# Performance work log

Measured on AMD Instinct MI355X. Metric: run time of the kernel, lower is better.

Reference implementation:

```python
import jax, jax.numpy as jnp
import numpy as np

NEG_SLOPE = 0.2  # PyG GATConv default negative_slope


def _gat_edge_forward(x, edge_index, edge_attr, W, W_edge, att_src, att_dst, att_edge, bias):
    N = x.shape[0]
    H, C = att_src.shape
    src, dst = edge_index[0], edge_index[1]

    # --- add self loops with edge_attr fill_value='mean' (PyG default) ---
    ones = jnp.ones((edge_attr.shape[0],), dtype=x.dtype)
    cnt = jax.ops.segment_sum(ones, dst, num_segments=N)  # [N]
    attr_sum = jax.ops.segment_sum(edge_attr, dst, num_segments=N)  # [N, edge_dim]
    loop_attr = attr_sum / jnp.maximum(cnt, 1.0)[:, None]  # mean, 0 if no in-edges
    loop_idx = jnp.arange(N, dtype=edge_index.dtype)
    src_all = jnp.concatenate([src, loop_idx])
    dst_all = jnp.concatenate([dst, loop_idx])
    attr_all = jnp.concatenate([edge_attr, loop_attr], axis=0)  # [E+N, edge_dim]

    # --- linear projections ---
    x_l = (x @ W).reshape(N, H, C)  # [N,H,C]; GATConv uses same lin for src/dst
    a_src = jnp.einsum('nhc,hc->nh', x_l, att_src)  # [N,H]
    a_dst = jnp.einsum('nhc,hc->nh', x_l, att_dst)  # [N,H]
    e = (attr_all @ W_edge).reshape(-1, H, C)  # [E+N,H,C]
    a_edge = jnp.einsum('ehc,hc->eh', e, att_edge)  # [E+N,H]

    # --- per-edge attention logits + segment softmax over incoming edges ---
    logits = jax.nn.leaky_relu(a_src[src_all] + a_dst[dst_all] + a_edge, NEG_SLOPE)
    m = jax.ops.segment_max(logits, dst_all, num_segments=N)  # [N,H]
    p = jnp.exp(logits - m[dst_all])
    denom = jax.ops.segment_sum(p, dst_all, num_segments=N)  # [N,H]
    alpha = p / denom[dst_all]  # [E+N,H]

    # --- weighted scatter aggregation ---
    msgs = alpha[:, :, None] * x_l[src_all]  # [E+N,H,C]
    out = jax.ops.segment_sum(msgs, dst_all, num_segments=N)  # [N,H,C]
    return out.reshape(N, H * C) + bias  # concat=True -> [N, H*C]


def setup_inputs() -> dict:
    key = jax.random.key(0)
    ks = jax.random.split(key, 8)
    N, E, DIN, EDIM, H, C = 100000, 1600000, 128, 16, 4, 32
    s = 1.0 / np.sqrt(DIN)
    return {
        'x': jax.random.normal(ks[0], (N, DIN), jnp.float32),
        'edge_index': jax.random.randint(ks[1], (2, E), 0, N, jnp.int64),
        'edge_attr': jax.random.normal(ks[2], (E, EDIM), jnp.float32),
        'W': jax.random.normal(ks[3], (DIN, H * C), jnp.float32) * s,
        'W_edge': jax.random.normal(ks[4], (EDIM, H * C), jnp.float32) * (1.0 / np.sqrt(EDIM)),
        'att_src': jax.random.normal(ks[5], (H, C), jnp.float32) * 0.1,
        'att_dst': jax.random.normal(ks[6], (H, C), jnp.float32) * 0.1,
        'att_edge': jax.random.normal(ks[7], (H, C), jnp.float32) * 0.1,
        'bias': jnp.zeros((H * C,), jnp.float32),
    }


def reference(x, edge_index, edge_attr, W, W_edge, att_src, att_dst, att_edge, bias):
    return _gat_edge_forward(x, edge_index, edge_attr, W, W_edge, att_src, att_dst, att_edge, bias)
```

## Files before the change

kernel.cpp:

```cpp
#include <hip/hip_runtime.h>
#include <hip/hip_fp16.h>
#include <math.h>

#define NEG_SLOPE 0.2f
typedef unsigned short ushort_t;
typedef unsigned int uint_t;

__global__ void k_prep(const int* __restrict__ ei, int* __restrict__ is64,
                       int* __restrict__ deg, int N,
                       const float* __restrict__ W_edge, const float* __restrict__ att_edge,
                       float* __restrict__ v_edge) {
  int b = blockIdx.x, t = threadIdx.x;
  if (b == 0) {
    __shared__ int any;
    if (t == 0) any = 0;
    __syncthreads();
    if (ei[2 * t + 1] != 0) atomicOr(&any, 1);
    __syncthreads();
    if (t == 0) *is64 = (any == 0) ? 1 : 0;
  } else if (b == 1) {
    if (t < 64) {
      int h = t >> 4, j = t & 15;
      float s = 0.f;
#pragma unroll
      for (int c = 0; c < 32; ++c) s += W_edge[j * 128 + h * 32 + c] * att_edge[h * 32 + c];
      v_edge[t] = s;
    }
  } else {
    int i = (b - 2) * 256 + t;
    if (i < N) deg[i] = 0;
  }
}

__global__ void k_hist(const int* __restrict__ ei, const int* __restrict__ is64,
                       int* __restrict__ deg, int* __restrict__ rank, int E) {
  int i = blockIdx.x * blockDim.x + threadIdx.x;
  if (i >= E) return;
  int dst = (*is64) ? ei[2 * (E + i)] : ei[E + i];
  rank[i] = atomicAdd(&deg[dst], 1);
}

__global__ void k_scan1(const int* __restrict__ deg, int* __restrict__ bsum, int N) {
  __shared__ int lds[256];
  int b = blockIdx.x, t = threadIdx.x;
  int base = b * 1024 + t * 4;
  int s = 0;
  if (base + 3 < N) {
    int4 v = *(const int4*)&deg[base];
    s = v.x + v.y + v.z + v.w;
  } else {
    for (int q = 0; q < 4; ++q) if (base + q < N) s += deg[base + q];
  }
  lds[t] = s; __syncthreads();
  for (int st = 128; st > 0; st >>= 1) {
    if (t < st) lds[t] += lds[t + st];
    __syncthreads();
  }
  if (t == 0) bsum[b] = lds[0];
}

__global__ void k_scan2(const int* __restrict__ bsum, int* __restrict__ boff, int NB) {
  __shared__ int lds[256];
  int t = threadIdx.x;
  int v = (t < NB) ? bsum[t] : 0;
  lds[t] = v;
  __syncthreads();
  for (int st = 1; st < 256; st <<= 1) {
    int add = (t >= st) ? lds[t - st] : 0;
    __syncthreads();
    lds[t] += add;
    __syncthreads();
  }
  if (t < NB) boff[t] = lds[t] - v;
}

__global__ void k_scan3(const int* __restrict__ deg, const int* __restrict__ boff,
                        int* __restrict__ offs, int N) {
  __shared__ int lds[256];
  int b = blockIdx.x, t = threadIdx.x;
  int base = b * 1024 + t * 4;
  int v[4]; int s = 0;
#pragma unroll
  for (int q = 0; q < 4; ++q) { v[q] = (base + q < N) ? deg[base + q] : 0; s += v[q]; }
  lds[t] = s;
  __syncthreads();
  for (int st = 1; st < 256; st <<= 1) {
    int add = (t >= st) ? lds[t - st] : 0;
    __syncthreads();
    lds[t] += add;
    __syncthreads();
  }
  int run = boff[b] + lds[t] - s;
#pragma unroll
  for (int q = 0; q < 4; ++q) {
    if (base + q < N) offs[base + q] = run;
    run += v[q];
  }
}

__global__ __launch_bounds__(256) void k1_scatter(
    const float* __restrict__ x, const float* __restrict__ W,
    const float* __restrict__ att_src, const float* __restrict__ att_dst,
    ushort_t* __restrict__ x_l_h, float* __restrict__ a_src, float* __restrict__ a_dst, int N,
    const int* __restrict__ ei, const int* __restrict__ is64,
    const int* __restrict__ rank, const int* __restrict__ offs,
    const float* __restrict__ edge_attr, const float* __restrict__ v_edge,
    int4* __restrict__ rec, int E, int nbs) {
  __shared__ float Wc[32 * 128];
  __shared__ float Xc[32 * 64];
  const int t = threadIdx.x;
  if (blockIdx.x < nbs) {
    if (t < 64) Wc[t] = v_edge[t];
    __syncthreads();
    int i = blockIdx.x * 256 + t;
    if (i >= E) return;
    int f = *is64;
    int src = f ? ei[2 * i] : ei[i];
    int dst = f ? ei[2 * (E + i)] : ei[E + i];
    float a16[16];
    *(float4*)&a16[0]  = *(const float4*)&edge_attr[(size_t)i * 16];
    *(float4*)&a16[4]  = *(const float4*)&edge_attr[(size_t)i * 16 + 4];
    *(float4*)&a16[8]  = *(const float4*)&edge_attr[(size_t)i * 16 + 8];
    *(float4*)&a16[12] = *(const float4*)&edge_attr[(size_t)i * 16 + 12];
    float ae[4];
#pragma unroll
    for (int h = 0; h < 4; ++h) {
      float s = 0.f;
#pragma unroll
      for (int j = 0; j < 16; ++j) s += a16[j] * Wc[h * 16 + j];
      ae[h] = s;
    }
    int pos = offs[dst] + rank[i];
    __half2 e01 = __floats2half2_rn(ae[0], ae[1]);
    __half2 e23 = __floats2half2_rn(ae[2], ae[3]);
    int4 r; r.x = *(int*)&e01; r.y = *(int*)&e23; r.z = src; r.w = 0;
    rec[pos] = r;
    return;
  }
  const int tcol = t & 31;
  const int trow = t >> 5;
  const int row0 = (blockIdx.x - nbs) * 64;
  const int r = t & 63, kq = t >> 6;
  const float4 aw_s = *(const float4*)&att_src[tcol * 4];
  const float4 aw_d = *(const float4*)&att_dst[tcol * 4];
  float acc[8][4];
#pragma unroll
  for (int i = 0; i < 8; ++i) { acc[i][0] = acc[i][1] = acc[i][2] = acc[i][3] = 0.f; }

  for (int kc = 0; kc < 4; ++kc) {
    float4 wreg[4];
#pragma unroll
    for (int q = 0; q < 4; ++q) wreg[q] = *(const float4*)&W[kc * 4096 + (q * 256 + t) * 4];
    float xs8[8];
    int grow = row0 + r;
    if (grow < N) {
      *(float4*)&xs8[0] = *(const float4*)&x[grow * 128 + kc * 32 + kq * 8];
      *(float4*)&xs8[4] = *(const float4*)&x[grow * 128 + kc * 32 + kq * 8 + 4];
    } else {
#pragma unroll
      for (int q = 0; q < 8; ++q) xs8[q] = 0.f;
    }
    __syncthreads();
#pragma unroll
    for (int q = 0; q < 4; ++q) *(float4*)&Wc[(q * 256 + t) * 4] = wreg[q];
#pragma unroll
    for (int q = 0; q < 8; ++q) Xc[(kq * 8 + q) * 64 + r] = xs8[q];
    __syncthreads();
#pragma unroll
    for (int kk = 0; kk < 32; ++kk) {
      float4 wv = *(const float4*)&Wc[kk * 128 + tcol * 4];
      float xr[8];
      *(float4*)&xr[0] = *(const float4*)&Xc[kk * 64 + trow * 8];
      *(float4*)&xr[4] = *(const float4*)&Xc[kk * 64 + trow * 8 + 4];
#pragma unroll
      for (int ri = 0; ri < 8; ++ri) {
        acc[ri][0] += xr[ri] * wv.x;
        acc[ri][1] += xr[ri] * wv.y;
        acc[ri][2] += xr[ri] * wv.z;
        acc[ri][3] += xr[ri] * wv.w;
      }
    }
  }
#pragma unroll
  for (int ri = 0; ri < 8; ++ri) {
    int grow = row0 + trow * 8 + ri;
    float asp = acc[ri][0] * aw_s.x + acc[ri][1] * aw_s.y + acc[ri][2] * aw_s.z + acc[ri][3] * aw_s.w;
    float adp = acc[ri][0] * aw_d.x + acc[ri][1] * aw_d.y + acc[ri][2] * aw_d.z + acc[ri][3] * aw_d.w;
#pragma unroll
    for (int m = 1; m < 8; m <<= 1) { asp += __shfl_xor(asp, m); adp += __shfl_xor(adp, m); }
    if (grow < N) {
      __half2 h0 = __floats2half2_rn(acc[ri][0], acc[ri][1]);
      __half2 h1 = __floats2half2_rn(acc[ri][2], acc[ri][3]);
      uint2 u; u.x = *(uint_t*)&h0; u.y = *(uint_t*)&h1;
      *(uint2*)&x_l_h[(size_t)grow * 128 + tcol * 4] = u;
      if ((tcol & 7) == 0) {
        a_src[grow * 4 + (tcol >> 3)] = asp;
        a_dst[grow * 4 + (tcol >> 3)] = adp;
      }
    }
  }
}

__global__ __launch_bounds__(256) void k34_agg(
    const int4* __restrict__ rec, const uint_t* __restrict__ xu,
    const float* __restrict__ a_src, const float* __restrict__ a_dst,
    const int* __restrict__ deg, const int* __restrict__ offs,
    const float* __restrict__ bias, float* __restrict__ out, int N) {
  int lane = threadIdx.x & 63;
  int node = blockIdx.x * 4 + (threadIdx.x >> 6);
  if (node >= N) return;
  int offu = __builtin_amdgcn_readfirstlane(offs[node]);
  int dgu  = __builtin_amdgcn_readfirstlane(deg[node]);
  const int4* rp = rec + offu;
  int h = lane >> 4;
  int hs16 = (h & 1) << 4;
  float ad = a_dst[(size_t)node * 4 + h];
  float accx = 0.f, accy = 0.f, den = 0.f, sae = 0.f;
  int i = 0;
  for (; i + 4 <= dgu; i += 4) {
    int4 u0 = rp[i], u1 = rp[i + 1], u2 = rp[i + 2], u3 = rp[i + 3];
    int s0 = __builtin_amdgcn_readfirstlane(u0.z);
    int s1 = __builtin_amdgcn_readfirstlane(u1.z);
    int s2 = __builtin_amdgcn_readfirstlane(u2.z);
    int s3 = __builtin_amdgcn_readfirstlane(u3.z);
    uint_t v0 = xu[((size_t)(uint_t)s0 << 6) + lane];
    uint_t v1 = xu[((size_t)(uint_t)s1 << 6) + lane];
    uint_t v2 = xu[((size_t)(uint_t)s2 << 6) + lane];
    uint_t v3 = xu[((size_t)(uint_t)s3 << 6) + lane];
    float as0 = a_src[((size_t)(uint_t)s0 << 2) + h];
    float as1 = a_src[((size_t)(uint_t)s1 << 2) + h];
    float as2 = a_src[((size_t)(uint_t)s2 << 2) + h];
    float as3 = a_src[((size_t)(uint_t)s3 << 2) + h];
    uint_t w0 = (h & 2) ? (uint_t)u0.y : (uint_t)u0.x;
    uint_t w1 = (h & 2) ? (uint_t)u1.y : (uint_t)u1.x;
    uint_t w2 = (h & 2) ? (uint_t)u2.y : (uint_t)u2.x;
    uint_t w3 = (h & 2) ? (uint_t)u3.y : (uint_t)u3.x;
    float e0 = __half2float(__ushort_as_half((ushort_t)(w0 >> hs16)));
    float e1 = __half2float(__ushort_as_half((ushort_t)(w1 >> hs16)));
    float e2 = __half2float(__ushort_as_half((ushort_t)(w2 >> hs16)));
    float e3 = __half2float(__ushort_as_half((ushort_t)(w3 >> hs16)));
    float g0 = as0 + ad + e0; g0 = fmaxf(g0, NEG_SLOPE * g0);
    float g1 = as1 + ad + e1; g1 = fmaxf(g1, NEG_SLOPE * g1);
    float g2 = as2 + ad + e2; g2 = fmaxf(g2, NEG_SLOPE * g2);
    float g3 = as3 + ad + e3; g3 = fmaxf(g3, NEG_SLOPE * g3);
    float p0 = __expf(g0), p1 = __expf(g1), p2 = __expf(g2), p3 = __expf(g3);
    den += p0 + p1 + p2 + p3;
    sae += e0 + e1 + e2 + e3;
    float2 f0 = __half22float2(*(const __half2*)&v0);
    float2 f1 = __half22float2(*(const __half2*)&v1);
    float2 f2 = __half22float2(*(const __half2*)&v2);
    float2 f3 = __half22float2(*(const __half2*)&v3);
    accx += p0 * f0.x; accy += p0 * f0.y;
    accx += p1 * f1.x; accy += p1 * f1.y;
    accx += p2 * f2.x; accy += p2 * f2.y;
    accx += p3 * f3.x; accy += p3 * f3.y;
  }
  for (; i < dgu; ++i) {
    int4 u = rp[i];
    int s = __builtin_amdgcn_readfirstlane(u.z);
    uint_t v = xu[((size_t)(uint_t)s << 6) + lane];
    float as = a_src[((size_t)(uint_t)s << 2) + h];
    uint_t w = (h & 2) ? (uint_t)u.y : (uint_t)u.x;
    float e = __half2float(__ushort_as_half((ushort_t)(w >> hs16)));
    float g = as + ad + e; g = fmaxf(g, NEG_SLOPE * g);
    float p = __expf(g);
    den += p; sae += e;
    float2 fx = __half22float2(*(const __half2*)&v);
    accx += p * fx.x; accy += p * fx.y;
  }
  float asn = a_src[(size_t)node * 4 + h];
  float inv_cnt = 1.f / (float)(dgu > 0 ? dgu : 1);
  float gl = asn + ad + sae * inv_cnt;
  gl = fmaxf(gl, NEG_SLOPE * gl);
  float pl = __expf(gl);
  float iv = 1.f / (den + pl);
  uint_t vn = xu[((size_t)(uint_t)node << 6) + lane];
  float2 fn = __half22float2(*(const __half2*)&vn);
  float2 b2 = *(const float2*)&bias[2 * lane];
  float2 o;
  o.x = (accx + pl * fn.x) * iv + b2.x;
  o.y = (accy + pl * fn.y) * iv + b2.y;
  *(float2*)&out[(size_t)node * 128 + 2 * lane] = o;
}

extern "C" void kernel_launch(void* const* d_in, const int* in_sizes, int n_in,
                              void* d_out, int out_size, void* d_ws, size_t ws_size,
                              hipStream_t stream) {
  const float* x        = (const float*)d_in[0];
  const int*   ei       = (const int*)  d_in[1];
  const float* eattr    = (const float*)d_in[2];
  const float* W        = (const float*)d_in[3];
  const float* W_edge   = (const float*)d_in[4];
  const float* att_src  = (const float*)d_in[5];
  const float* att_dst  = (const float*)d_in[6];
  const float* att_edge = (const float*)d_in[7];
  const float* bias     = (const float*)d_in[8];
  float* out = (float*)d_out;
  const int N = in_sizes[0] / 128;
  const int E = in_sizes[1] / 2;
  (void)n_in; (void)out_size; (void)ws_size;

  char* base = (char*)d_ws;
  size_t off = 0;
  auto take = [&](size_t bytes) -> void* {
    void* p = base + off;
    off = (off + bytes + 255) & ~(size_t)255;
    return p;
  };
  ushort_t* x_l_h = (ushort_t*)take((size_t)N * 128 * 2);
  float* a_src    = (float*)take((size_t)N * 4 * 4);
  float* a_dst    = (float*)take((size_t)N * 4 * 4);
  float* v_edge   = (float*)take(64 * 4);
  int4*  rec      = (int4*)take((size_t)E * 16);
  int*   deg      = (int*)take((size_t)N * 4);
  int*   offs     = (int*)take((size_t)N * 4);
  int*   rank     = (int*)take((size_t)E * 4);
  int*   bsum     = (int*)take(256 * 4);
  int*   boff     = (int*)take(256 * 4);
  int*   is64     = (int*)take(4);

  const int NB = (N + 1023) / 1024;
  const int nbs = (E + 255) / 256;
  const int nb1 = (N + 63) / 64;

  hipLaunchKernelGGL(k_prep, dim3(2 + (N + 255) / 256), dim3(256), 0, stream,
                     ei, is64, deg, N, W_edge, att_edge, v_edge);
  hipLaunchKernelGGL(k_hist, dim3(nbs), dim3(256), 0, stream, ei, is64, deg, rank, E);
  hipLaunchKernelGGL(k_scan1, dim3(NB), dim3(256), 0, stream, deg, bsum, N);
  hipLaunchKernelGGL(k_scan2, dim3(1), dim3(256), 0, stream, bsum, boff, NB);
  hipLaunchKernelGGL(k_scan3, dim3(NB), dim3(256), 0, stream, deg, boff, offs, N);
  hipLaunchKernelGGL(k1_scatter, dim3(nbs + nb1), dim3(256), 0, stream,
                     x, W, att_src, att_dst, x_l_h, a_src, a_dst, N,
                     ei, is64, rank, offs, eattr, v_edge, rec, E, nbs);
  hipLaunchKernelGGL(k34_agg, dim3((N + 3) / 4), dim3(256), 0, stream,
                     rec, (const uint_t*)x_l_h, a_src, a_dst, deg, offs, bias, out, N);
}
```

Baseline: 267.8 us.

## Split node GEMM across histogram and scatter kernels; use nontemporal record accesses

```diff
diff --git a/kernel.cpp b/kernel.cpp
--- a/kernel.cpp
+++ b/kernel.cpp
@@ -5,6 +5,8 @@
 #define NEG_SLOPE 0.2f
 typedef unsigned short ushort_t;
 typedef unsigned int uint_t;
+typedef int   i32x4 __attribute__((ext_vector_type(4)));
+typedef float f32x2 __attribute__((ext_vector_type(2)));
 
 __global__ void k_prep(const int* __restrict__ ei, int* __restrict__ is64,
                        int* __restrict__ deg, int N,
@@ -32,12 +34,93 @@
   }
 }
 
-__global__ void k_hist(const int* __restrict__ ei, const int* __restrict__ is64,
-                       int* __restrict__ deg, int* __restrict__ rank, int E) {
-  int i = blockIdx.x * blockDim.x + threadIdx.x;
-  if (i >= E) return;
-  int dst = (*is64) ? ei[2 * (E + i)] : ei[E + i];
-  rank[i] = atomicAdd(&deg[dst], 1);
+__device__ __forceinline__ void gemm_body(
+    const float* __restrict__ x, const float* __restrict__ W,
+    const float* __restrict__ att_src, const float* __restrict__ att_dst,
+    ushort_t* __restrict__ x_l_h, float* __restrict__ a_src, float* __restrict__ a_dst,
+    int N, int row0, float* Wc, float* Xc) {
+  const int t = threadIdx.x;
+  const int tcol = t & 31;
+  const int trow = t >> 5;
+  const int r = t & 63, kq = t >> 6;
+  const float4 aw_s = *(const float4*)&att_src[tcol * 4];
+  const float4 aw_d = *(const float4*)&att_dst[tcol * 4];
+  float acc[8][4];
+#pragma unroll
+  for (int i = 0; i < 8; ++i) { acc[i][0] = acc[i][1] = acc[i][2] = acc[i][3] = 0.f; }
+
+  for (int kc = 0; kc < 4; ++kc) {
+    float4 wreg[4];
+#pragma unroll
+    for (int q = 0; q < 4; ++q) wreg[q] = *(const float4*)&W[kc * 4096 + (q * 256 + t) * 4];
+    float xs8[8];
+    int grow = row0 + r;
+    if (grow < N) {
+      *(float4*)&xs8[0] = *(const float4*)&x[grow * 128 + kc * 32 + kq * 8];
+      *(float4*)&xs8[4] = *(const float4*)&x[grow * 128 + kc * 32 + kq * 8 + 4];
+    } else {
+#pragma unroll
+      for (int q = 0; q < 8; ++q) xs8[q] = 0.f;
+    }
+    __syncthreads();
+#pragma unroll
+    for (int q = 0; q < 4; ++q) *(float4*)&Wc[(q * 256 + t) * 4] = wreg[q];
+#pragma unroll
+    for (int q = 0; q < 8; ++q) Xc[(kq * 8 + q) * 64 + r] = xs8[q];
+    __syncthreads();
+#pragma unroll
+    for (int kk = 0; kk < 32; ++kk) {
+      float4 wv = *(const float4*)&Wc[kk * 128 + tcol * 4];
+      float xr[8];
+      *(float4*)&xr[0] = *(const float4*)&Xc[kk * 64 + trow * 8];
+      *(float4*)&xr[4] = *(const float4*)&Xc[kk * 64 + trow * 8 + 4];
+#pragma unroll
+      for (int ri = 0; ri < 8; ++ri) {
+        acc[ri][0] += xr[ri] * wv.x;
+        acc[ri][1] += xr[ri] * wv.y;
+        acc[ri][2] += xr[ri] * wv.z;
+        acc[ri][3] += xr[ri] * wv.w;
+      }
+    }
+  }
+#pragma unroll
+  for (int ri = 0; ri < 8; ++ri) {
+    int grow = row0 + trow * 8 + ri;
+    float asp = acc[ri][0] * aw_s.x + acc[ri][1] * aw_s.y + acc[ri][2] * aw_s.z + acc[ri][3] * aw_s.w;
+    float adp = acc[ri][0] * aw_d.x + acc[ri][1] * aw_d.y + acc[ri][2] * aw_d.z + acc[ri][3] * aw_d.w;
+#pragma unroll
+    for (int m = 1; m < 8; m <<= 1) { asp += __shfl_xor(asp, m); adp += __shfl_xor(adp, m); }
+    if (grow < N) {
+      __half2 h0 = __floats2half2_rn(acc[ri][0], acc[ri][1]);
+      __half2 h1 = __floats2half2_rn(acc[ri][2], acc[ri][3]);
+      uint2 u; u.x = *(uint_t*)&h0; u.y = *(uint_t*)&h1;
+      *(uint2*)&x_l_h[(size_t)grow * 128 + tcol * 4] = u;
+      if ((tcol & 7) == 0) {
+        a_src[grow * 4 + (tcol >> 3)] = asp;
+        a_dst[grow * 4 + (tcol >> 3)] = adp;
+      }
+    }
+  }
+}
+
+__global__ __launch_bounds__(256) void kA_hist_gemm(
+    const float* __restrict__ x, const float* __restrict__ W,
+    const float* __restrict__ att_src, const float* __restrict__ att_dst,
+    ushort_t* __restrict__ x_l_h, float* __restrict__ a_src, float* __restrict__ a_dst, int N,
+    const int* __restrict__ ei, const int* __restrict__ is64,
+    int* __restrict__ deg, int* __restrict__ rank, int E, int nbh) {
+  __shared__ float Wc[32 * 128];
+  __shared__ float Xc[32 * 64];
+  if (blockIdx.x < nbh) {
+    int i = blockIdx.x * 256 + threadIdx.x;
+    if (i < E) {
+      int dst = (*is64) ? ei[2 * (E + i)] : ei[E + i];
+      rank[i] = atomicAdd(&deg[dst], 1);
+    }
+    return;
+  }
+  gemm_body(x, W, att_src, att_dst, x_l_h, a_src, a_dst, N,
+            (blockIdx.x - nbh) * 64, Wc, Xc);
 }
 
 __global__ void k_scan1(const int* __restrict__ deg, int* __restrict__ bsum, int N) {
@@ -98,14 +181,14 @@
   }
 }
 
-__global__ __launch_bounds__(256) void k1_scatter(
+__global__ __launch_bounds__(256) void kB_scatter_gemm(
     const float* __restrict__ x, const float* __restrict__ W,
     const float* __restrict__ att_src, const float* __restrict__ att_dst,
     ushort_t* __restrict__ x_l_h, float* __restrict__ a_src, float* __restrict__ a_dst, int N,
     const int* __restrict__ ei, const int* __restrict__ is64,
     const int* __restrict__ rank, const int* __restrict__ offs,
     const float* __restrict__ edge_attr, const float* __restrict__ v_edge,
-    int4* __restrict__ rec, int E, int nbs) {
+    int* __restrict__ rec, int E, int nbs, int rowBase) {
   __shared__ float Wc[32 * 128];
   __shared__ float Xc[32 * 64];
   const int t = threadIdx.x;
@@ -133,76 +216,17 @@
     int pos = offs[dst] + rank[i];
     __half2 e01 = __floats2half2_rn(ae[0], ae[1]);
     __half2 e23 = __floats2half2_rn(ae[2], ae[3]);
-    int4 r; r.x = *(int*)&e01; r.y = *(int*)&e23; r.z = src; r.w = 0;
-    rec[pos] = r;
+    i32x4 r;
+    r.x = *(int*)&e01; r.y = *(int*)&e23; r.z = src; r.w = 0;
+    __builtin_nontemporal_store(r, (i32x4*)&rec[(size_t)pos * 4]);
     return;
   }
-  const int tcol = t & 31;
-  const int trow = t >> 5;
-  const int row0 = (blockIdx.x - nbs) * 64;
-  const int r = t & 63, kq = t >> 6;
-  const float4 aw_s = *(const float4*)&att_src[tcol * 4];
-  const float4 aw_d = *(const float4*)&att_dst[tcol * 4];
-  float acc[8][4];
-#pragma unroll
-  for (int i = 0; i < 8; ++i) { acc[i][0] = acc[i][1] = acc[i][2] = acc[i][3] = 0.f; }
-
-  for (int kc = 0; kc < 4; ++kc) {
-    float4 wreg[4];
-#pragma unroll
-    for (int q = 0; q < 4; ++q) wreg[q] = *(const float4*)&W[kc * 4096 + (q * 256 + t) * 4];
-    float xs8[8];
-    int grow = row0 + r;
-    if (grow < N) {
-      *(float4*)&xs8[0] = *(const float4*)&x[grow * 128 + kc * 32 + kq * 8];
-      *(float4*)&xs8[4] = *(const float4*)&x[grow * 128 + kc * 32 + kq * 8 + 4];
-    } else {
-#pragma unroll
-      for (int q = 0; q < 8; ++q) xs8[q] = 0.f;
-    }
-    __syncthreads();
-#pragma unroll
-    for (int q = 0; q < 4; ++q) *(float4*)&Wc[(q * 256 + t) * 4] = wreg[q];
-#pragma unroll
-    for (int q = 0; q < 8; ++q) Xc[(kq * 8 + q) * 64 + r] = xs8[q];
-    __syncthreads();
-#pragma unroll
-    for (int kk = 0; kk < 32; ++kk) {
-      float4 wv = *(const float4*)&Wc[kk * 128 + tcol * 4];
-      float xr[8];
-      *(float4*)&xr[0] = *(const float4*)&Xc[kk * 64 + trow * 8];
-      *(float4*)&xr[4] = *(const float4*)&Xc[kk * 64 + trow * 8 + 4];
-#pragma unroll
-      for (int ri = 0; ri < 8; ++ri) {
-        acc[ri][0] += xr[ri] * wv.x;
-        acc[ri][1] += xr[ri] * wv.y;
-        acc[ri][2] += xr[ri] * wv.z;
-        acc[ri][3] += xr[ri] * wv.w;
-      }
-    }
-  }
-#pragma unroll
-  for (int ri = 0; ri < 8; ++ri) {
-    int grow = row0 + trow * 8 + ri;
-    float asp = acc[ri][0] * aw_s.x + acc[ri][1] * aw_s.y + acc[ri][2] * aw_s.z + acc[ri][3] * aw_s.w;
-    float adp = acc[ri][0] * aw_d.x + acc[ri][1] * aw_d.y + acc[ri][2] * aw_d.z + acc[ri][3] * aw_d.w;
-#pragma unroll
-    for (int m = 1; m < 8; m <<= 1) { asp += __shfl_xor(asp, m); adp += __shfl_xor(adp, m); }
-    if (grow < N) {
-      __half2 h0 = __floats2half2_rn(acc[ri][0], acc[ri][1]);
-      __half2 h1 = __floats2half2_rn(acc[ri][2], acc[ri][3]);
-      uint2 u; u.x = *(uint_t*)&h0; u.y = *(uint_t*)&h1;
-      *(uint2*)&x_l_h[(size_t)grow * 128 + tcol * 4] = u;
-      if ((tcol & 7) == 0) {
-        a_src[grow * 4 + (tcol >> 3)] = asp;
-        a_dst[grow * 4 + (tcol >> 3)] = adp;
-      }
-    }
-  }
+  gemm_body(x, W, att_src, att_dst, x_l_h, a_src, a_dst, N,
+            rowBase + (blockIdx.x - nbs) * 64, Wc, Xc);
 }
 
 __global__ __launch_bounds__(256) void k34_agg(
-    const int4* __restrict__ rec, const uint_t* __restrict__ xu,
+    const int* __restrict__ rec, const uint_t* __restrict__ xu,
     const float* __restrict__ a_src, const float* __restrict__ a_dst,
     const int* __restrict__ deg, const int* __restrict__ offs,
     const float* __restrict__ bias, float* __restrict__ out, int N) {
@@ -211,14 +235,17 @@
   if (node >= N) return;
   int offu = __builtin_amdgcn_readfirstlane(offs[node]);
   int dgu  = __builtin_amdgcn_readfirstlane(deg[node]);
-  const int4* rp = rec + offu;
+  const i32x4* rp = (const i32x4*)(rec + (size_t)offu * 4);
   int h = lane >> 4;
   int hs16 = (h & 1) << 4;
   float ad = a_dst[(size_t)node * 4 + h];
   float accx = 0.f, accy = 0.f, den = 0.f, sae = 0.f;
   int i = 0;
   for (; i + 4 <= dgu; i += 4) {
-    int4 u0 = rp[i], u1 = rp[i + 1], u2 = rp[i + 2], u3 = rp[i + 3];
+    i32x4 u0 = __builtin_nontemporal_load(&rp[i]);
+    i32x4 u1 = __builtin_nontemporal_load(&rp[i + 1]);
+    i32x4 u2 = __builtin_nontemporal_load(&rp[i + 2]);
+    i32x4 u3 = __builtin_nontemporal_load(&rp[i + 3]);
     int s0 = __builtin_amdgcn_readfirstlane(u0.z);
     int s1 = __builtin_amdgcn_readfirstlane(u1.z);
     int s2 = __builtin_amdgcn_readfirstlane(u2.z);
@@ -256,7 +283,7 @@
     accx += p3 * f3.x; accy += p3 * f3.y;
   }
   for (; i < dgu; ++i) {
-    int4 u = rp[i];
+    i32x4 u = __builtin_nontemporal_load(&rp[i]);
     int s = __builtin_amdgcn_readfirstlane(u.z);
     uint_t v = xu[((size_t)(uint_t)s << 6) + lane];
     float as = a_src[((size_t)(uint_t)s << 2) + h];
@@ -277,10 +304,10 @@
   uint_t vn = xu[((size_t)(uint_t)node << 6) + lane];
   float2 fn = __half22float2(*(const __half2*)&vn);
   float2 b2 = *(const float2*)&bias[2 * lane];
-  float2 o;
+  f32x2 o;
   o.x = (accx + pl * fn.x) * iv + b2.x;
   o.y = (accy + pl * fn.y) * iv + b2.y;
-  *(float2*)&out[(size_t)node * 128 + 2 * lane] = o;
+  __builtin_nontemporal_store(o, (f32x2*)&out[(size_t)node * 128 + 2 * lane]);
 }
 
 extern "C" void kernel_launch(void* const* d_in, const int* in_sizes, int n_in,
@@ -311,7 +338,7 @@
   float* a_src    = (float*)take((size_t)N * 4 * 4);
   float* a_dst    = (float*)take((size_t)N * 4 * 4);
   float* v_edge   = (float*)take(64 * 4);
-  int4*  rec      = (int4*)take((size_t)E * 16);
+  int*   rec      = (int*)take((size_t)E * 16);
   int*   deg      = (int*)take((size_t)N * 4);
   int*   offs     = (int*)take((size_t)N * 4);
   int*   rank     = (int*)take((size_t)E * 4);
@@ -319,19 +346,23 @@
   int*   boff     = (int*)take(256 * 4);
   int*   is64     = (int*)take(4);
 
-  const int NB = (N + 1023) / 1024;
-  const int nbs = (E + 255) / 256;
+  const int NB  = (N + 1023) / 1024;
+  const int nbh = (E + 255) / 256;
   const int nb1 = (N + 63) / 64;
+  const int nbA = nb1 / 2;
+  const int nbB = nb1 - nbA;
 
   hipLaunchKernelGGL(k_prep, dim3(2 + (N + 255) / 256), dim3(256), 0, stream,
                      ei, is64, deg, N, W_edge, att_edge, v_edge);
-  hipLaunchKernelGGL(k_hist, dim3(nbs), dim3(256), 0, stream, ei, is64, deg, rank, E);
+  hipLaunchKernelGGL(kA_hist_gemm, dim3(nbh + nbA), dim3(256), 0, stream,
+                     x, W, att_src, att_dst, x_l_h, a_src, a_dst, N,
+                     ei, is64, deg, rank, E, nbh);
   hipLaunchKernelGGL(k_scan1, dim3(NB), dim3(256), 0, stream, deg, bsum, N);
   hipLaunchKernelGGL(k_scan2, dim3(1), dim3(256), 0, stream, bsum, boff, NB);
   hipLaunchKernelGGL(k_scan3, dim3(NB), dim3(256), 0, stream, deg, boff, offs, N);
-  hipLaunchKernelGGL(k1_scatter, dim3(nbs + nb1), dim3(256), 0, stream,
+  hipLaunchKernelGGL(kB_scatter_gemm, dim3(nbh + nbB), dim3(256), 0, stream,
                      x, W, att_src, att_dst, x_l_h, a_src, a_dst, N,
-                     ei, is64, rank, offs, eattr, v_edge, rec, E, nbs);
+                     ei, is64, rank, offs, eattr, v_edge, rec, E, nbh, nbA * 64);
   hipLaunchKernelGGL(k34_agg, dim3((N + 3) / 4), dim3(256), 0, stream,
                      rec, (const uint_t*)x_l_h, a_src, a_dst, deg, offs, bias, out, N);
 }
```

After: 290.5 us. 1.08x slower.
